# Optimization experiments

Measured on AMD Instinct MI355X. Metric: run time of the kernel, lower is better.

Reference implementation:

```python
import jax, jax.numpy as jnp
import numpy as np

H = W = 2048
C = 8
N = 1_000_000


def setup_inputs() -> dict:
    key = jax.random.key(0)
    k1, k2 = jax.random.split(key)
    # coords in [0, H-4); the forward's mod wraps any value into range anyway
    coords = jax.random.uniform(k1, (N, 2), dtype=jnp.float32) * (H - 4)
    visible = jax.random.normal(k2, (H, W, C), dtype=jnp.float32)
    return {"coords": coords, "visible": visible}


def reference(coords, visible):
    dims = jnp.asarray(visible.shape[:2], dtype=coords.dtype)  # [2] = (H, W)
    # wrap coordinates into [1, dim-3) exactly like the TF layer
    c = ((coords - 1.0) % (dims - 4.0)) + 1.0          # [N,2]
    idx_low = jnp.floor(c)
    delta = c - idx_low                                 # [N,2]
    i = idx_low.astype(jnp.int32)                       # [N,2]

    def g(di, dj):  # gather visible at idx_low + [di, dj] -> [N,C]
        return visible[i[:, 0] + di, i[:, 1] + dj]

    top_left, top_right = g(0, 0), g(1, 0)
    bottom_left, bottom_right = g(0, 1), g(1, 1)

    d0 = delta[:, :1]   # delta along first coord axis, [N,1]
    d1 = delta[:, 1:2]  # delta along second coord axis, [N,1]

    mid_bottom = bottom_right + d0 * (bottom_left - bottom_right)
    mid_top = top_right + d0 * (top_left - top_right)
    interpolation = mid_bottom + d1 * (mid_top - mid_bottom)  # [N,C]

    # boundary mask exactly as in source (compares only coord 0; mod makes it a no-op)
    off = c > dims                                       # [N,2]
    cond = jnp.logical_or(off[:, 0], off[:, 0])          # [N]
    return jnp.where(cond[:, None], jnp.zeros_like(interpolation), interpolation)
```

## Files before the change

### kernel.cpp

```cpp
#include <hip/hip_runtime.h>

#define HH 2048
#define WW 2048
#define CC 8
#define MODV 2044.0f

typedef float f32x2 __attribute__((ext_vector_type(2)));
typedef float f32x4 __attribute__((ext_vector_type(4)));

__device__ __forceinline__ f32x4 blerp4(f32x4 tl, f32x4 tr, f32x4 bl, f32x4 br,
                                        float d0, float d1, float m) {
    f32x4 mb = br + d0 * (bl - br);
    f32x4 mt = tr + d0 * (tl - tr);
    return m * (mb + d1 * (mt - mb));
}

__device__ __forceinline__ const float* point_addr(f32x2 co, const float* visible,
                                                   float& d0, float& d1, float& m) {
    float x = co.x - 1.0f;
    float y = co.y - 1.0f;
    float cx = fmodf(x, MODV); if (cx < 0.0f) cx += MODV;
    float cy = fmodf(y, MODV); if (cy < 0.0f) cy += MODV;
    cx += 1.0f;
    cy += 1.0f;
    float fx = floorf(cx);
    float fy = floorf(cy);
    d0 = cx - fx;
    d1 = cy - fy;
    int i0 = (int)fx;
    int i1 = (int)fy;
    m = (cx > (float)HH) ? 0.0f : 1.0f;
    return visible + ((size_t)i0 * WW + (size_t)i1) * CC;
}

__global__ __launch_bounds__(256, 5) void idx2pixel_kernel(
    const float* __restrict__ coords,
    const float* __restrict__ visible,
    float* __restrict__ out,
    int n)
{
    int t = blockIdx.x * blockDim.x + threadIdx.x;
    int half = (n + 1) >> 1;
    if (t >= half) return;
    int tB = t + half;
    bool hB = tB < n;
    int iB = hB ? tB : t;

    const f32x2* cp = reinterpret_cast<const f32x2*>(coords);
    f32x2 coA = cp[t];
    f32x2 coB = cp[iB];

    float d0A, d1A, mA, d0B, d1B, mB;
    const float* pA = point_addr(coA, visible, d0A, d1A, mA);
    const float* pB = point_addr(coB, visible, d0B, d1B, mB);
    const size_t RS = (size_t)WW * CC;

#define LD8(P, base)                                   \
    f32x4 P##tl0 = *(const f32x4*)(base);              \
    f32x4 P##tl1 = *(const f32x4*)((base) + 4);        \
    f32x4 P##bl0 = *(const f32x4*)((base) + 8);        \
    f32x4 P##bl1 = *(const f32x4*)((base) + 12);       \
    f32x4 P##tr0 = *(const f32x4*)((base) + RS);       \
    f32x4 P##tr1 = *(const f32x4*)((base) + RS + 4);   \
    f32x4 P##br0 = *(const f32x4*)((base) + RS + 8);   \
    f32x4 P##br1 = *(const f32x4*)((base) + RS + 12);

    LD8(A, pA)
    LD8(B, pB)
#undef LD8

    __builtin_amdgcn_sched_barrier(0);

    {
        f32x4 o0 = blerp4(Atl0, Atr0, Abl0, Abr0, d0A, d1A, mA);
        f32x4 o1 = blerp4(Atl1, Atr1, Abl1, Abr1, d0A, d1A, mA);
        float* po = out + (size_t)t * CC;
        *(f32x4*)po = o0;
        *(f32x4*)(po + 4) = o1;
    }
    {
        f32x4 o0 = blerp4(Btl0, Btr0, Bbl0, Bbr0, d0B, d1B, mB);
        f32x4 o1 = blerp4(Btl1, Btr1, Bbl1, Bbr1, d0B, d1B, mB);
        if (hB) {
            float* po = out + (size_t)tB * CC;
            *(f32x4*)po = o0;
            *(f32x4*)(po + 4) = o1;
        }
    }
}

extern "C" void kernel_launch(void* const* d_in, const int* in_sizes, int n_in,
                              void* d_out, int out_size, void* d_ws, size_t ws_size,
                              hipStream_t stream) {
    const float* coords  = (const float*)d_in[0];
    const float* visible = (const float*)d_in[1];
    float* out = (float*)d_out;
    int n = in_sizes[0] / 2;

    int half = (n + 1) >> 1;
    int block = 256;
    int grid = (half + block - 1) / block;
    idx2pixel_kernel<<<grid, block, 0, stream>>>(coords, visible, out, n);
}
```

Baseline: 225.7 us.

## Bin points by row band and pin bands to XCDs for cache locality

```diff
diff --git a/kernel.cpp b/kernel.cpp
--- a/kernel.cpp
+++ b/kernel.cpp
@@ -4,6 +4,8 @@
 #define WW 2048
 #define CC 8
 #define MODV 2044.0f
+#define NB 128
+#define BAND_SHIFT 4
 
 typedef float f32x2 __attribute__((ext_vector_type(2)));
 typedef float f32x4 __attribute__((ext_vector_type(4)));
@@ -15,78 +17,130 @@
     return m * (mb + d1 * (mt - mb));
 }
 
-__device__ __forceinline__ const float* point_addr(f32x2 co, const float* visible,
-                                                   float& d0, float& d1, float& m) {
+__device__ __forceinline__ void mod_coords(f32x2 co, float& cx, float& cy) {
     float x = co.x - 1.0f;
     float y = co.y - 1.0f;
-    float cx = fmodf(x, MODV); if (cx < 0.0f) cx += MODV;
-    float cy = fmodf(y, MODV); if (cy < 0.0f) cy += MODV;
-    cx += 1.0f;
-    cy += 1.0f;
+    cx = fmodf(x, MODV); if (cx < 0.0f) cx += MODV; cx += 1.0f;
+    cy = fmodf(y, MODV); if (cy < 0.0f) cy += MODV; cy += 1.0f;
+}
+
+__device__ __forceinline__ void interp_store(const float* __restrict__ visible,
+                                             float* __restrict__ out,
+                                             float cx, float cy, unsigned oi) {
     float fx = floorf(cx);
     float fy = floorf(cy);
-    d0 = cx - fx;
-    d1 = cy - fy;
+    float d0 = cx - fx;
+    float d1 = cy - fy;
     int i0 = (int)fx;
     int i1 = (int)fy;
-    m = (cx > (float)HH) ? 0.0f : 1.0f;
-    return visible + ((size_t)i0 * WW + (size_t)i1) * CC;
+    float m = (cx > (float)HH) ? 0.0f : 1.0f;
+
+    const float* p = visible + ((size_t)i0 * WW + (size_t)i1) * CC;
+    const size_t RS = (size_t)WW * CC;
+    f32x4 tl0 = *(const f32x4*)(p);
+    f32x4 tl1 = *(const f32x4*)(p + 4);
+    f32x4 bl0 = *(const f32x4*)(p + 8);
+    f32x4 bl1 = *(const f32x4*)(p + 12);
+    f32x4 tr0 = *(const f32x4*)(p + RS);
+    f32x4 tr1 = *(const f32x4*)(p + RS + 4);
+    f32x4 br0 = *(const f32x4*)(p + RS + 8);
+    f32x4 br1 = *(const f32x4*)(p + RS + 12);
+
+    f32x4 o0 = blerp4(tl0, tr0, bl0, br0, d0, d1, m);
+    f32x4 o1 = blerp4(tl1, tr1, bl1, br1, d0, d1, m);
+    float* po = out + (size_t)oi * CC;
+    *(f32x4*)po = o0;
+    *(f32x4*)(po + 4) = o1;
 }
 
-__global__ __launch_bounds__(256, 5) void idx2pixel_kernel(
+__global__ void zero_cnt(unsigned* __restrict__ cnt) {
+    cnt[threadIdx.x] = 0u;
+}
+
+__global__ __launch_bounds__(1024) void bin_points(
     const float* __restrict__ coords,
     const float* __restrict__ visible,
     float* __restrict__ out,
-    int n)
+    unsigned* __restrict__ cnt,
+    float* __restrict__ rcx, float* __restrict__ rcy,
+    unsigned* __restrict__ ridx,
+    int n, int cap)
+{
+    __shared__ unsigned lcnt[NB];
+    __shared__ unsigned lbase[NB];
+    int tid = threadIdx.x;
+    if (tid < NB) lcnt[tid] = 0u;
+    __syncthreads();
+
+    int i = blockIdx.x * 1024 + tid;
+    bool valid = i < n;
+    float cx = 1.0f, cy = 1.0f;
+    int key = 0;
+    unsigned lr = 0;
+    if (valid) {
+        f32x2 co = reinterpret_cast<const f32x2*>(coords)[i];
+        mod_coords(co, cx, cy);
+        int i0 = (int)floorf(cx);
+        int band = (i0 - 1) >> BAND_SHIFT;
+        key = ((band & 7) << 4) | (band >> 3);
+        lr = atomicAdd(&lcnt[key], 1u);
+    }
+    __syncthreads();
+    if (tid < NB && lcnt[tid]) lbase[tid] = atomicAdd(&cnt[tid], lcnt[tid]);
+    __syncthreads();
+    if (valid) {
+        unsigned p = lbase[key] + lr;
+        if (p < (unsigned)cap) {
+            int slot = key * cap + (int)p;
+            rcx[slot] = cx;
+            rcy[slot] = cy;
+            ridx[slot] = (unsigned)i;
+        } else {
+            interp_store(visible, out, cx, cy, (unsigned)i);
+        }
+    }
+}
+
+__global__ __launch_bounds__(256) void gather_binned(
+    const float* __restrict__ visible,
+    float* __restrict__ out,
+    const unsigned* __restrict__ cnt,
+    const float* __restrict__ rcx, const float* __restrict__ rcy,
+    const unsigned* __restrict__ ridx,
+    int cap)
+{
+    const int tslots = (NB / 8) * cap;
+    int xcd = blockIdx.x & 7;
+    int j   = blockIdx.x >> 3;
+    int nbx = gridDim.x >> 3;
+    int base = xcd * tslots;
+
+    for (int s0 = j * 256; s0 < tslots; s0 += nbx * 256) {
+        int slot = base + s0 + threadIdx.x;
+        int bin = slot / cap;
+        int r = slot - bin * cap;
+        unsigned cb = cnt[bin];
+        if (cb > (unsigned)cap) cb = (unsigned)cap;
+        if ((unsigned)r < cb) {
+            float cx = rcx[slot];
+            float cy = rcy[slot];
+            unsigned oi = ridx[slot];
+            interp_store(visible, out, cx, cy, oi);
+        }
+    }
+}
+
+__global__ __launch_bounds__(256) void idx2pixel_direct(
+    const float* __restrict__ coords,
+    const float* __restrict__ visible,
+    float* __restrict__ out, int n)
 {
     int t = blockIdx.x * blockDim.x + threadIdx.x;
-    int half = (n + 1) >> 1;
-    if (t >= half) return;
-    int tB = t + half;
-    bool hB = tB < n;
-    int iB = hB ? tB : t;
-
-    const f32x2* cp = reinterpret_cast<const f32x2*>(coords);
-    f32x2 coA = cp[t];
-    f32x2 coB = cp[iB];
-
-    float d0A, d1A, mA, d0B, d1B, mB;
-    const float* pA = point_addr(coA, visible, d0A, d1A, mA);
-    const float* pB = point_addr(coB, visible, d0B, d1B, mB);
-    const size_t RS = (size_t)WW * CC;
-
-#define LD8(P, base)                                   \
-    f32x4 P##tl0 = *(const f32x4*)(base);              \
-    f32x4 P##tl1 = *(const f32x4*)((base) + 4);        \
-    f32x4 P##bl0 = *(const f32x4*)((base) + 8);        \
-    f32x4 P##bl1 = *(const f32x4*)((base) + 12);       \
-    f32x4 P##tr0 = *(const f32x4*)((base) + RS);       \
-    f32x4 P##tr1 = *(const f32x4*)((base) + RS + 4);   \
-    f32x4 P##br0 = *(const f32x4*)((base) + RS + 8);   \
-    f32x4 P##br1 = *(const f32x4*)((base) + RS + 12);
-
-    LD8(A, pA)
-    LD8(B, pB)
-#undef LD8
-
-    __builtin_amdgcn_sched_barrier(0);
-
-    {
-        f32x4 o0 = blerp4(Atl0, Atr0, Abl0, Abr0, d0A, d1A, mA);
-        f32x4 o1 = blerp4(Atl1, Atr1, Abl1, Abr1, d0A, d1A, mA);
-        float* po = out + (size_t)t * CC;
-        *(f32x4*)po = o0;
-        *(f32x4*)(po + 4) = o1;
-    }
-    {
-        f32x4 o0 = blerp4(Btl0, Btr0, Bbl0, Bbr0, d0B, d1B, mB);
-        f32x4 o1 = blerp4(Btl1, Btr1, Bbl1, Bbr1, d0B, d1B, mB);
-        if (hB) {
-            float* po = out + (size_t)tB * CC;
-            *(f32x4*)po = o0;
-            *(f32x4*)(po + 4) = o1;
-        }
-    }
+    if (t >= n) return;
+    f32x2 co = reinterpret_cast<const f32x2*>(coords)[t];
+    float cx, cy;
+    mod_coords(co, cx, cy);
+    interp_store(visible, out, cx, cy, (unsigned)t);
 }
 
 extern "C" void kernel_launch(void* const* d_in, const int* in_sizes, int n_in,
@@ -97,8 +151,27 @@
     float* out = (float*)d_out;
     int n = in_sizes[0] / 2;
 
-    int half = (n + 1) >> 1;
-    int block = 256;
-    int grid = (half + block - 1) / block;
-    idx2pixel_kernel<<<grid, block, 0, stream>>>(coords, visible, out, n);
+    int mean = (n + NB - 1) / NB;
+    int margin = mean / 8 + 1024;
+    int cap = (mean + margin + 255) & ~255;
+    size_t slots = (size_t)NB * (size_t)cap;
+    size_t need = 1024 + slots * 12;
+
+    if (ws_size >= need && n >= (1 << 17)) {
+        unsigned* cnt = (unsigned*)d_ws;
+        float* rcx = (float*)((char*)d_ws + 1024);
+        float* rcy = rcx + slots;
+        unsigned* ridx = (unsigned*)(rcy + slots);
+
+        zero_cnt<<<1, NB, 0, stream>>>(cnt);
+        int nb1 = (n + 1023) / 1024;
+        bin_points<<<nb1, 1024, 0, stream>>>(coords, visible, out, cnt,
+                                             rcx, rcy, ridx, n, cap);
+        gather_binned<<<2048, 256, 0, stream>>>(visible, out, cnt,
+                                                rcx, rcy, ridx, cap);
+    } else {
+        int block = 256;
+        int grid = (n + block - 1) / block;
+        idx2pixel_direct<<<grid, block, 0, stream>>>(coords, visible, out, n);
+    }
 }
```

Measured after the change: 282.8 us. +25.3%, slower.
